# Kernel tuning notes

Hardware: AMD Instinct MI355X
Metric: run time of the kernel (lower is better)

Reference implementation:

```python
import jax, jax.numpy as jnp
import numpy as np

TOP_K = 2


def setup_inputs() -> dict:
    key = jax.random.key(0)
    k0, k1, k2, k3, k4 = jax.random.split(key, 5)
    B, S, D, E, F = 4, 2048, 1024, 8, 512
    return {
        "hidden_states": jax.random.normal(k0, (B, S, D), dtype=jnp.float32),
        "router_weight": jax.random.normal(k1, (E, D), dtype=jnp.float32) * 0.02,
        "w_gate": jax.random.normal(k2, (E, D, F), dtype=jnp.float32) * 0.02,
        "w_up": jax.random.normal(k3, (E, D, F), dtype=jnp.float32) * 0.02,
        "w_down": jax.random.normal(k4, (E, F, D), dtype=jnp.float32) * 0.02,
    }


def reference(hidden_states, router_weight, w_gate, w_up, w_down):
    B, S, D = hidden_states.shape
    E = router_weight.shape[0]
    x = hidden_states.reshape(-1, D)          # [T, D] token-flattened
    T = x.shape[0]

    # --- TopKRouter: softmax over experts, top-k, renormalize selected probs ---
    logits = x @ router_weight.T              # [T, E]
    probs = jax.nn.softmax(logits, axis=-1)
    top_p, top_i = jax.lax.top_k(probs, TOP_K)            # [T, k]
    top_p = top_p / jnp.sum(top_p, axis=-1, keepdims=True)  # renormalize=True

    # combine weights: scatter selected probabilities into [T, E]
    combine = jnp.zeros((T, E), x.dtype).at[jnp.arange(T)[:, None], top_i].add(top_p)

    # --- Grouped SwiGLU experts (dropless: zero combine weight => zero contribution) ---
    g = jnp.einsum('td,edf->tef', x, w_gate)  # [T, E, F]
    u = jnp.einsum('td,edf->tef', x, w_up)    # [T, E, F]
    h = jax.nn.silu(g) * u                    # SwiGLU activation
    # down-proj + weighted combine fused
    out = jnp.einsum('tef,efd,te->td', h, w_down, combine)  # [T, D]
    return out.reshape(B, S, D)
```

## Files before the change

kernel.cpp:

```cpp
#include <hip/hip_runtime.h>
#include <hip/hip_bf16.h>


typedef __attribute__((ext_vector_type(4))) float  f32x4;
typedef __attribute__((ext_vector_type(8))) unsigned short us8;
typedef __attribute__((ext_vector_type(4))) unsigned short us4;
typedef __bf16 bf16_t;
typedef __attribute__((ext_vector_type(8))) bf16_t bf16x8;

#define TTOK 8192
#define DDIM 1024
#define EEXP 8
#define FDIM 512

__device__ __forceinline__ unsigned short f2bf(float f) {
  unsigned int u = __float_as_uint(f);
  u = (u + 0x7FFFu + ((u >> 16) & 1u)) >> 16;
  return (unsigned short)u;
}

__device__ __forceinline__ void gload16(const void* g, void* l) {
  __builtin_amdgcn_global_load_lds(
      (const __attribute__((address_space(1))) void*)g,
      (__attribute__((address_space(3))) void*)l, 16, 0, 0);
}

__global__ __launch_bounds__(256) void k_cvt_x(const float* __restrict__ x,
                                               unsigned short* __restrict__ xb) {
  int i = blockIdx.x * 256 + threadIdx.x;
  const f32x4* s = (const f32x4*)x + (size_t)i * 2;
  f32x4 a = s[0], b = s[1];
  us8 o;
  o[0]=f2bf(a[0]); o[1]=f2bf(a[1]); o[2]=f2bf(a[2]); o[3]=f2bf(a[3]);
  o[4]=f2bf(b[0]); o[5]=f2bf(b[1]); o[6]=f2bf(b[2]); o[7]=f2bf(b[3]);
  *((us8*)xb + i) = o;
}

__global__ __launch_bounds__(256) void k_tcvt(const float* __restrict__ src,
                                              unsigned short* __restrict__ dst,
                                              int M, int N) {
  __shared__ float tile[32][33];
  int e  = blockIdx.z;
  int m0 = blockIdx.y * 32, n0 = blockIdx.x * 32;
  const float* s = src + (size_t)e * M * N;
  unsigned short* d = dst + (size_t)e * M * N;
  int r  = threadIdx.x >> 3;
  int c4 = (threadIdx.x & 7) * 4;
  f32x4 v = *(const f32x4*)(s + (size_t)(m0 + r) * N + n0 + c4);
  tile[r][c4+0] = v[0]; tile[r][c4+1] = v[1];
  tile[r][c4+2] = v[2]; tile[r][c4+3] = v[3];
  __syncthreads();
  us4 o;
  o[0] = f2bf(tile[c4+0][r]); o[1] = f2bf(tile[c4+1][r]);
  o[2] = f2bf(tile[c4+2][r]); o[3] = f2bf(tile[c4+3][r]);
  *(us4*)(d + (size_t)(n0 + r) * M + m0 + c4) = o;
}

__global__ __launch_bounds__(256) void k_router(const float* __restrict__ x,
                                                const float* __restrict__ rw,
                                                int* __restrict__ topki,
                                                float* __restrict__ topkw) {
  __shared__ float wlds[8 * 1024];
  int tid = threadIdx.x;
  #pragma unroll
  for (int i = 0; i < 8; ++i)
    ((f32x4*)wlds)[tid + i * 256] = ((const f32x4*)rw)[tid + i * 256];
  __syncthreads();

  int wv = tid >> 6, lane = tid & 63;
  int t = blockIdx.x * 4 + wv;
  const f32x4* xr = (const f32x4*)(x + (size_t)t * DDIM);
  f32x4 xv[4];
  #pragma unroll
  for (int j = 0; j < 4; ++j) xv[j] = xr[j * 64 + lane];
  double xd[16];
  #pragma unroll
  for (int j = 0; j < 4; ++j) {
    xd[j*4+0] = xv[j][0]; xd[j*4+1] = xv[j][1];
    xd[j*4+2] = xv[j][2]; xd[j*4+3] = xv[j][3];
  }
  float pf[8];
  #pragma unroll
  for (int e = 0; e < 8; ++e) {
    double acc = 0.0;
    #pragma unroll
    for (int j = 0; j < 4; ++j) {
      f32x4 wv4 = ((const f32x4*)(wlds + e * 1024))[j * 64 + lane];
      acc = fma((double)wv4[0], xd[j*4+0], acc);
      acc = fma((double)wv4[1], xd[j*4+1], acc);
      acc = fma((double)wv4[2], xd[j*4+2], acc);
      acc = fma((double)wv4[3], xd[j*4+3], acc);
    }
    pf[e] = (float)acc;
  }
  #pragma unroll
  for (int e = 0; e < 8; ++e) {
    #pragma unroll
    for (int off = 32; off >= 1; off >>= 1)
      pf[e] += __shfl_xor(pf[e], off, 64);
  }
  if (lane == 0) {
    int i1 = 0;
    #pragma unroll
    for (int e2 = 1; e2 < 8; ++e2) if (pf[e2] > pf[i1]) i1 = e2;
    int i2 = (i1 == 0) ? 1 : 0;
    #pragma unroll
    for (int e2 = 0; e2 < 8; ++e2) if (e2 != i1 && pf[e2] > pf[i2]) i2 = e2;
    float d21 = pf[i2] - pf[i1];
    float e1  = __expf(d21);
    float s   = 1.f + e1;
    topki[2*t]   = i1;       topki[2*t+1] = i2;
    topkw[2*t]   = 1.f / s;  topkw[2*t+1] = e1 / s;
  }
}

__global__ __launch_bounds__(256) void k_count(const int* __restrict__ topki,
                                               int* __restrict__ ctrs) {
  __shared__ int h[8];
  if (threadIdx.x < 8) h[threadIdx.x] = 0;
  __syncthreads();
  int i = blockIdx.x * 256 + threadIdx.x;
  atomicAdd(&h[topki[i]], 1);
  __syncthreads();
  if (threadIdx.x < 8) atomicAdd(&ctrs[threadIdx.x], h[threadIdx.x]);
}

__global__ void k_scan(int* __restrict__ ctrs) {
  if (threadIdx.x == 0 && blockIdx.x == 0) {
    ctrs[8] = 0;
    #pragma unroll
    for (int e = 0; e < 8; ++e) ctrs[9 + e] = ctrs[8 + e] + ctrs[e];
    #pragma unroll
    for (int e = 0; e < 8; ++e) ctrs[17 + e] = 0;
  }
}

__global__ __launch_bounds__(256) void k_scatter(const int* __restrict__ topki,
                                                 const float* __restrict__ topkw,
                                                 int* __restrict__ ctrs,
                                                 int* __restrict__ at,
                                                 float* __restrict__ aw) {
  __shared__ int lc[8], base[8];
  int tid = threadIdx.x;
  if (tid < 8) lc[tid] = 0;
  __syncthreads();
  int t = blockIdx.x * 256 + tid;
  int e0 = topki[2*t], e1 = topki[2*t+1];
  int r0 = atomicAdd(&lc[e0], 1);
  int r1 = atomicAdd(&lc[e1], 1);
  __syncthreads();
  if (tid < 8) base[tid] = atomicAdd(&ctrs[17 + tid], lc[tid]);
  __syncthreads();
  int a0 = ctrs[8 + e0] + base[e0] + r0;
  int a1 = ctrs[8 + e1] + base[e1] + r1;
  at[a0] = t; aw[a0] = topkw[2*t];
  at[a1] = t; aw[a1] = topkw[2*t+1];
}

__global__ __launch_bounds__(256) void k_gateup(
    const unsigned short* __restrict__ xb,
    const unsigned short* __restrict__ wgt,
    const unsigned short* __restrict__ wut,
    const int* __restrict__ at,
    const int* __restrict__ ctrs,
    unsigned short* __restrict__ h) {
  int e    = blockIdx.z;
  int seg0 = ctrs[8 + e];
  int cnt  = ctrs[9 + e] - seg0;
  int row0 = blockIdx.y * 128;
  if (row0 >= cnt) return;
  int f0 = blockIdx.x * 128;

  __shared__ unsigned short lA [128 * 64];
  __shared__ unsigned short lBg[128 * 64];
  __shared__ unsigned short lBu[128 * 64];
  __shared__ int s_tok[128];

  int tid = threadIdx.x;
  if (tid < 128) {
    int rg = row0 + tid;
    s_tok[tid] = at[seg0 + ((rg < cnt) ? rg : 0)];
  }
  __syncthreads();

  int a_row[4], a_su[4];
  const unsigned short* aSrc[4];
  size_t bOff[4];
  #pragma unroll
  for (int i = 0; i < 4; ++i) {
    a_row[i] = i * 32 + (tid >> 3);
    a_su[i]  = (tid & 7) ^ (a_row[i] & 7);
    aSrc[i]  = xb + (size_t)s_tok[a_row[i]] * DDIM + a_su[i] * 8;
    bOff[i]  = (size_t)a_row[i] * DDIM + a_su[i] * 8;
  }
  const unsigned short* bgBase = wgt + ((size_t)e * FDIM + f0) * DDIM;
  const unsigned short* buBase = wut + ((size_t)e * FDIM + f0) * DDIM;

  int w = tid >> 6, lane = tid & 63;
  int wr = (w >> 1) * 64, wc = (w & 1) * 64;

  f32x4 zero = {0.f, 0.f, 0.f, 0.f};
  f32x4 accg[4][4], accu[4][4];
  #pragma unroll
  for (int mt = 0; mt < 4; ++mt)
    #pragma unroll
    for (int nt = 0; nt < 4; ++nt) { accg[mt][nt] = zero; accu[mt][nt] = zero; }

  for (int ks = 0; ks < DDIM / 64; ++ks) {
    int k0 = ks * 64;
    #pragma unroll
    for (int i = 0; i < 4; ++i) {
      int dst = (i * 256 + tid) * 8;
      gload16(aSrc[i] + k0,          &lA [dst]);
      gload16(bgBase + bOff[i] + k0, &lBg[dst]);
      gload16(buBase + bOff[i] + k0, &lBu[dst]);
    }
    __syncthreads();
    #pragma unroll
    for (int kk = 0; kk < 2; ++kk) {
      bf16x8 af[4];
      #pragma unroll
      for (int mt = 0; mt < 4; ++mt) {
        int ar = wr + mt * 16 + (lane & 15);
        int au = (kk * 4 + (lane >> 4)) ^ (ar & 7);
        af[mt] = *(const bf16x8*)&lA[(ar * 8 + au) * 8];
      }
      #pragma unroll
      for (int nt = 0; nt < 4; ++nt) {
        int br = wc + nt * 16 + (lane & 15);
        int bu = (kk * 4 + (lane >> 4)) ^ (br & 7);
        bf16x8 bg = *(const bf16x8*)&lBg[(br * 8 + bu) * 8];
        bf16x8 bv = *(const bf16x8*)&lBu[(br * 8 + bu) * 8];
        #pragma unroll
        for (int mt = 0; mt < 4; ++mt) {
          accg[mt][nt] = __builtin_amdgcn_mfma_f32_16x16x32_bf16(af[mt], bg, accg[mt][nt], 0, 0, 0);
          accu[mt][nt] = __builtin_amdgcn_mfma_f32_16x16x32_bf16(af[mt], bv, accu[mt][nt], 0, 0, 0);
        }
      }
    }
    __syncthreads();
  }
  #pragma unroll
  for (int mt = 0; mt < 4; ++mt) {
    #pragma unroll
    for (int nt = 0; nt < 4; ++nt) {
      #pragma unroll
      for (int j = 0; j < 4; ++j) {
        int rl = wr + mt * 16 + (lane >> 4) * 4 + j;
        if (row0 + rl < cnt) {
          float g = accg[mt][nt][j], u = accu[mt][nt][j];
          float hv = g * (1.f / (1.f + __expf(-g))) * u;
          h[(size_t)(seg0 + row0 + rl) * FDIM + f0 + wc + nt * 16 + (lane & 15)] = f2bf(hv);
        }
      }
    }
  }
}

__global__ __launch_bounds__(256) void k_down(
    const unsigned short* __restrict__ h,
    const unsigned short* __restrict__ wdt,
    const int* __restrict__ at,
    const float* __restrict__ aw,
    const int* __restrict__ ctrs,
    float* __restrict__ out) {
  int e    = blockIdx.z;
  int seg0 = ctrs[8 + e];
  int cnt  = ctrs[9 + e] - seg0;
  int row0 = blockIdx.y * 128;
  if (row0 >= cnt) return;
  int d0 = blockIdx.x * 128;

  __shared__ unsigned short lA[128 * 64];
  __shared__ unsigned short lB[128 * 64];
  __shared__ int   s_tok[128];
  __shared__ float s_w[128];

  int tid = threadIdx.x;
  if (tid < 128) {
    int rg = row0 + tid;
    int a  = seg0 + ((rg < cnt) ? rg : 0);
    s_tok[tid] = at[a];
    s_w[tid]   = aw[a];
  }

  int a_row[4], a_su[4];
  const unsigned short* aSrc[4];
  size_t bOff[4];
  #pragma unroll
  for (int i = 0; i < 4; ++i) {
    a_row[i] = i * 32 + (tid >> 3);
    a_su[i]  = (tid & 7) ^ (a_row[i] & 7);
    int rr   = (row0 + a_row[i] < cnt) ? row0 + a_row[i] : 0;
    aSrc[i]  = h + (size_t)(seg0 + rr) * FDIM + a_su[i] * 8;
    bOff[i]  = (size_t)a_row[i] * FDIM + a_su[i] * 8;
  }
  const unsigned short* bBase = wdt + ((size_t)e * DDIM + d0) * FDIM;

  int w = tid >> 6, lane = tid & 63;
  int wr = (w >> 1) * 64, wc = (w & 1) * 64;

  f32x4 zero = {0.f, 0.f, 0.f, 0.f};
  f32x4 acc[4][4];
  #pragma unroll
  for (int mt = 0; mt < 4; ++mt)
    #pragma unroll
    for (int nt = 0; nt < 4; ++nt) acc[mt][nt] = zero;

  for (int ks = 0; ks < FDIM / 64; ++ks) {
    int k0 = ks * 64;
    #pragma unroll
    for (int i = 0; i < 4; ++i) {
      int dst = (i * 256 + tid) * 8;
      gload16(aSrc[i] + k0,         &lA[dst]);
      gload16(bBase + bOff[i] + k0, &lB[dst]);
    }
    __syncthreads();
    #pragma unroll
    for (int kk = 0; kk < 2; ++kk) {
      bf16x8 af[4];
      #pragma unroll
      for (int mt = 0; mt < 4; ++mt) {
        int ar = wr + mt * 16 + (lane & 15);
        int au = (kk * 4 + (lane >> 4)) ^ (ar & 7);
        af[mt] = *(const bf16x8*)&lA[(ar * 8 + au) * 8];
      }
      #pragma unroll
      for (int nt = 0; nt < 4; ++nt) {
        int br = wc + nt * 16 + (lane & 15);
        int bu = (kk * 4 + (lane >> 4)) ^ (br & 7);
        bf16x8 bf = *(const bf16x8*)&lB[(br * 8 + bu) * 8];
        #pragma unroll
        for (int mt = 0; mt < 4; ++mt)
          acc[mt][nt] = __builtin_amdgcn_mfma_f32_16x16x32_bf16(af[mt], bf, acc[mt][nt], 0, 0, 0);
      }
    }
    __syncthreads();
  }
  #pragma unroll
  for (int mt = 0; mt < 4; ++mt) {
    #pragma unroll
    for (int nt = 0; nt < 4; ++nt) {
      #pragma unroll
      for (int j = 0; j < 4; ++j) {
        int rl = wr + mt * 16 + (lane >> 4) * 4 + j;
        if (row0 + rl < cnt) {
          float v = acc[mt][nt][j] * s_w[rl];
          atomicAdd(out + (size_t)s_tok[rl] * DDIM + d0 + wc + nt * 16 + (lane & 15), v);
        }
      }
    }
  }
}

extern "C" void kernel_launch(void* const* d_in, const int* in_sizes, int n_in,
                              void* d_out, int out_size, void* d_ws, size_t ws_size,
                              hipStream_t stream) {
  (void)in_sizes; (void)n_in; (void)ws_size;
  const float* x  = (const float*)d_in[0];
  const float* rw = (const float*)d_in[1];
  const float* wg = (const float*)d_in[2];
  const float* wu = (const float*)d_in[3];
  const float* wd = (const float*)d_in[4];
  float* out = (float*)d_out;

  char* ws = (char*)d_ws;
  unsigned short* xb  = (unsigned short*)(ws + 0);
  unsigned short* wgt = (unsigned short*)(ws + 16777216);
  unsigned short* wut = (unsigned short*)(ws + 25165824);
  unsigned short* wdt = (unsigned short*)(ws + 33554432);
  unsigned short* hbuf= (unsigned short*)(ws + 41943040);
  float* topkw = (float*)(ws + 58720256);
  int*   topki = (int*)  (ws + 58785792);
  int*   at    = (int*)  (ws + 58851328);
  float* aw    = (float*)(ws + 58916864);
  int*   ctrs  = (int*)  (ws + 58982400);

  hipMemsetAsync(ctrs, 0, 256, stream);
  hipMemsetAsync(out, 0, (size_t)out_size * sizeof(float), stream);

  k_cvt_x<<<4096, 256, 0, stream>>>(x, xb);
  k_tcvt <<<dim3(16, 32, 8), 256, 0, stream>>>(wg, wgt, 1024, 512);
  k_tcvt <<<dim3(16, 32, 8), 256, 0, stream>>>(wu, wut, 1024, 512);
  k_tcvt <<<dim3(32, 16, 8), 256, 0, stream>>>(wd, wdt, 512, 1024);
  k_router<<<2048, 256, 0, stream>>>(x, rw, topki, topkw);
  k_count <<<64, 256, 0, stream>>>(topki, ctrs);
  k_scan  <<<1, 64, 0, stream>>>(ctrs);
  k_scatter<<<32, 256, 0, stream>>>(topki, topkw, ctrs, at, aw);
  k_gateup<<<dim3(4, 128, 8), 256, 0, stream>>>(xb, wgt, wut, at, ctrs, hbuf);
  k_down  <<<dim3(8, 128, 8), 256, 0, stream>>>(hbuf, wdt, at, aw, ctrs, out);
}
```

Baseline: 323.7 us.

## Double-buffer LDS and enlarge tiles in grouped MoE GEMM kernels

Both expert GEMM kernels now use 512-thread blocks with 256-row tiles (and 256-column tiles in the down projection), plus double-buffered LDS. The next K-slice is prefetched while the current one is computed, which removes one barrier per iteration and hides global-load latency. The larger tiles improve weight reuse across tokens. The cost is much higher LDS use (about 128KB per block in k_down), more accumulator registers per thread, lower occupancy and more wasted work on partially filled expert tiles.

After: 306.2 us. 5.4% less time.

```diff
diff --git a/kernel.cpp b/kernel.cpp
--- a/kernel.cpp
+++ b/kernel.cpp
@@ -157,7 +157,7 @@
   at[a1] = t; aw[a1] = topkw[2*t+1];
 }
 
-__global__ __launch_bounds__(256) void k_gateup(
+__global__ __launch_bounds__(512, 2) void k_gateup(
     const unsigned short* __restrict__ xb,
     const unsigned short* __restrict__ wgt,
     const unsigned short* __restrict__ wut,
@@ -167,31 +167,35 @@
   int e    = blockIdx.z;
   int seg0 = ctrs[8 + e];
   int cnt  = ctrs[9 + e] - seg0;
-  int row0 = blockIdx.y * 128;
+  int row0 = blockIdx.y * 256;
   if (row0 >= cnt) return;
   int f0 = blockIdx.x * 128;
 
-  __shared__ unsigned short lA [128 * 64];
-  __shared__ unsigned short lBg[128 * 64];
-  __shared__ unsigned short lBu[128 * 64];
-  __shared__ int s_tok[128];
+  __shared__ unsigned short lA [2][256 * 64];
+  __shared__ unsigned short lBg[2][128 * 64];
+  __shared__ unsigned short lBu[2][128 * 64];
+  __shared__ int s_tok[256];
 
   int tid = threadIdx.x;
-  if (tid < 128) {
+  if (tid < 256) {
     int rg = row0 + tid;
     s_tok[tid] = at[seg0 + ((rg < cnt) ? rg : 0)];
   }
   __syncthreads();
 
-  int a_row[4], a_su[4];
   const unsigned short* aSrc[4];
-  size_t bOff[4];
+  size_t bOff[2];
   #pragma unroll
   for (int i = 0; i < 4; ++i) {
-    a_row[i] = i * 32 + (tid >> 3);
-    a_su[i]  = (tid & 7) ^ (a_row[i] & 7);
-    aSrc[i]  = xb + (size_t)s_tok[a_row[i]] * DDIM + a_su[i] * 8;
-    bOff[i]  = (size_t)a_row[i] * DDIM + a_su[i] * 8;
+    int row = i * 64 + (tid >> 3);
+    int su  = (tid & 7) ^ (row & 7);
+    aSrc[i] = xb + (size_t)s_tok[row] * DDIM + su * 8;
+  }
+  #pragma unroll
+  for (int j = 0; j < 2; ++j) {
+    int row = j * 64 + (tid >> 3);
+    int su  = (tid & 7) ^ (row & 7);
+    bOff[j] = (size_t)row * DDIM + su * 8;
   }
   const unsigned short* bgBase = wgt + ((size_t)e * FDIM + f0) * DDIM;
   const unsigned short* buBase = wut + ((size_t)e * FDIM + f0) * DDIM;
@@ -206,16 +210,28 @@
     #pragma unroll
     for (int nt = 0; nt < 4; ++nt) { accg[mt][nt] = zero; accu[mt][nt] = zero; }
 
+  #pragma unroll
+  for (int i = 0; i < 4; ++i) gload16(aSrc[i], &lA[0][(i * 512 + tid) * 8]);
+  #pragma unroll
+  for (int j = 0; j < 2; ++j) {
+    gload16(bgBase + bOff[j], &lBg[0][(j * 512 + tid) * 8]);
+    gload16(buBase + bOff[j], &lBu[0][(j * 512 + tid) * 8]);
+  }
+  __syncthreads();
+
+  int cur = 0;
   for (int ks = 0; ks < DDIM / 64; ++ks) {
-    int k0 = ks * 64;
-    #pragma unroll
-    for (int i = 0; i < 4; ++i) {
-      int dst = (i * 256 + tid) * 8;
-      gload16(aSrc[i] + k0,          &lA [dst]);
-      gload16(bgBase + bOff[i] + k0, &lBg[dst]);
-      gload16(buBase + bOff[i] + k0, &lBu[dst]);
-    }
-    __syncthreads();
+    if (ks + 1 < DDIM / 64) {
+      int k1 = (ks + 1) * 64;
+      int nx = cur ^ 1;
+      #pragma unroll
+      for (int i = 0; i < 4; ++i) gload16(aSrc[i] + k1, &lA[nx][(i * 512 + tid) * 8]);
+      #pragma unroll
+      for (int j = 0; j < 2; ++j) {
+        gload16(bgBase + bOff[j] + k1, &lBg[nx][(j * 512 + tid) * 8]);
+        gload16(buBase + bOff[j] + k1, &lBu[nx][(j * 512 + tid) * 8]);
+      }
+    }
     #pragma unroll
     for (int kk = 0; kk < 2; ++kk) {
       bf16x8 af[4];
@@ -223,14 +239,14 @@
       for (int mt = 0; mt < 4; ++mt) {
         int ar = wr + mt * 16 + (lane & 15);
         int au = (kk * 4 + (lane >> 4)) ^ (ar & 7);
-        af[mt] = *(const bf16x8*)&lA[(ar * 8 + au) * 8];
+        af[mt] = *(const bf16x8*)&lA[cur][(ar * 8 + au) * 8];
       }
       #pragma unroll
       for (int nt = 0; nt < 4; ++nt) {
         int br = wc + nt * 16 + (lane & 15);
         int bu = (kk * 4 + (lane >> 4)) ^ (br & 7);
-        bf16x8 bg = *(const bf16x8*)&lBg[(br * 8 + bu) * 8];
-        bf16x8 bv = *(const bf16x8*)&lBu[(br * 8 + bu) * 8];
+        bf16x8 bg = *(const bf16x8*)&lBg[cur][(br * 8 + bu) * 8];
+        bf16x8 bv = *(const bf16x8*)&lBu[cur][(br * 8 + bu) * 8];
         #pragma unroll
         for (int mt = 0; mt < 4; ++mt) {
           accg[mt][nt] = __builtin_amdgcn_mfma_f32_16x16x32_bf16(af[mt], bg, accg[mt][nt], 0, 0, 0);
@@ -239,6 +255,7 @@
       }
     }
     __syncthreads();
+    cur ^= 1;
   }
   #pragma unroll
   for (int mt = 0; mt < 4; ++mt) {
@@ -257,7 +274,7 @@
   }
 }
 
-__global__ __launch_bounds__(256) void k_down(
+__global__ __launch_bounds__(512, 2) void k_down(
     const unsigned short* __restrict__ h,
     const unsigned short* __restrict__ wdt,
     const int* __restrict__ at,
@@ -267,55 +284,64 @@
   int e    = blockIdx.z;
   int seg0 = ctrs[8 + e];
   int cnt  = ctrs[9 + e] - seg0;
-  int row0 = blockIdx.y * 128;
+  int row0 = blockIdx.y * 256;
   if (row0 >= cnt) return;
-  int d0 = blockIdx.x * 128;
-
-  __shared__ unsigned short lA[128 * 64];
-  __shared__ unsigned short lB[128 * 64];
-  __shared__ int   s_tok[128];
-  __shared__ float s_w[128];
+  int d0 = blockIdx.x * 256;
+
+  __shared__ unsigned short lA[2][256 * 64];
+  __shared__ unsigned short lB[2][256 * 64];
+  __shared__ int   s_tok[256];
+  __shared__ float s_w[256];
 
   int tid = threadIdx.x;
-  if (tid < 128) {
+  if (tid < 256) {
     int rg = row0 + tid;
     int a  = seg0 + ((rg < cnt) ? rg : 0);
     s_tok[tid] = at[a];
     s_w[tid]   = aw[a];
   }
-
-  int a_row[4], a_su[4];
+  __syncthreads();
+
   const unsigned short* aSrc[4];
   size_t bOff[4];
   #pragma unroll
   for (int i = 0; i < 4; ++i) {
-    a_row[i] = i * 32 + (tid >> 3);
-    a_su[i]  = (tid & 7) ^ (a_row[i] & 7);
-    int rr   = (row0 + a_row[i] < cnt) ? row0 + a_row[i] : 0;
-    aSrc[i]  = h + (size_t)(seg0 + rr) * FDIM + a_su[i] * 8;
-    bOff[i]  = (size_t)a_row[i] * FDIM + a_su[i] * 8;
+    int row = i * 64 + (tid >> 3);
+    int su  = (tid & 7) ^ (row & 7);
+    int rr  = (row0 + row < cnt) ? row0 + row : 0;
+    aSrc[i] = h + (size_t)(seg0 + rr) * FDIM + su * 8;
+    bOff[i] = (size_t)row * FDIM + su * 8;
   }
   const unsigned short* bBase = wdt + ((size_t)e * DDIM + d0) * FDIM;
 
   int w = tid >> 6, lane = tid & 63;
-  int wr = (w >> 1) * 64, wc = (w & 1) * 64;
+  int wr = (w >> 1) * 64, wc = (w & 1) * 128;
 
   f32x4 zero = {0.f, 0.f, 0.f, 0.f};
-  f32x4 acc[4][4];
+  f32x4 acc[4][8];
   #pragma unroll
   for (int mt = 0; mt < 4; ++mt)
     #pragma unroll
-    for (int nt = 0; nt < 4; ++nt) acc[mt][nt] = zero;
-
+    for (int nt = 0; nt < 8; ++nt) acc[mt][nt] = zero;
+
+  #pragma unroll
+  for (int i = 0; i < 4; ++i) {
+    gload16(aSrc[i],         &lA[0][(i * 512 + tid) * 8]);
+    gload16(bBase + bOff[i], &lB[0][(i * 512 + tid) * 8]);
+  }
+  __syncthreads();
+
+  int cur = 0;
   for (int ks = 0; ks < FDIM / 64; ++ks) {
-    int k0 = ks * 64;
-    #pragma unroll
-    for (int i = 0; i < 4; ++i) {
-      int dst = (i * 256 + tid) * 8;
-      gload16(aSrc[i] + k0,         &lA[dst]);
-      gload16(bBase + bOff[i] + k0, &lB[dst]);
-    }
-    __syncthreads();
+    if (ks + 1 < FDIM / 64) {
+      int k1 = (ks + 1) * 64;
+      int nx = cur ^ 1;
+      #pragma unroll
+      for (int i = 0; i < 4; ++i) {
+        gload16(aSrc[i] + k1,         &lA[nx][(i * 512 + tid) * 8]);
+        gload16(bBase + bOff[i] + k1, &lB[nx][(i * 512 + tid) * 8]);
+      }
+    }
     #pragma unroll
     for (int kk = 0; kk < 2; ++kk) {
       bf16x8 af[4];
@@ -323,24 +349,25 @@
       for (int mt = 0; mt < 4; ++mt) {
         int ar = wr + mt * 16 + (lane & 15);
         int au = (kk * 4 + (lane >> 4)) ^ (ar & 7);
-        af[mt] = *(const bf16x8*)&lA[(ar * 8 + au) * 8];
-      }
-      #pragma unroll
-      for (int nt = 0; nt < 4; ++nt) {
+        af[mt] = *(const bf16x8*)&lA[cur][(ar * 8 + au) * 8];
+      }
+      #pragma unroll
+      for (int nt = 0; nt < 8; ++nt) {
         int br = wc + nt * 16 + (lane & 15);
         int bu = (kk * 4 + (lane >> 4)) ^ (br & 7);
-        bf16x8 bf = *(const bf16x8*)&lB[(br * 8 + bu) * 8];
+        bf16x8 bf = *(const bf16x8*)&lB[cur][(br * 8 + bu) * 8];
         #pragma unroll
         for (int mt = 0; mt < 4; ++mt)
           acc[mt][nt] = __builtin_amdgcn_mfma_f32_16x16x32_bf16(af[mt], bf, acc[mt][nt], 0, 0, 0);
       }
     }
     __syncthreads();
+    cur ^= 1;
   }
   #pragma unroll
   for (int mt = 0; mt < 4; ++mt) {
     #pragma unroll
-    for (int nt = 0; nt < 4; ++nt) {
+    for (int nt = 0; nt < 8; ++nt) {
       #pragma unroll
       for (int j = 0; j < 4; ++j) {
         int rl = wr + mt * 16 + (lane >> 4) * 4 + j;
@@ -387,6 +414,6 @@
   k_count <<<64, 256, 0, stream>>>(topki, ctrs);
   k_scan  <<<1, 64, 0, stream>>>(ctrs);
   k_scatter<<<32, 256, 0, stream>>>(topki, topkw, ctrs, at, aw);
-  k_gateup<<<dim3(4, 128, 8), 256, 0, stream>>>(xb, wgt, wut, at, ctrs, hbuf);
-  k_down  <<<dim3(8, 128, 8), 256, 0, stream>>>(hbuf, wdt, at, aw, ctrs, out);
-}
+  k_gateup<<<dim3(4, 64, 8), 512, 0, stream>>>(xb, wgt, wut, at, ctrs, hbuf);
+  k_down  <<<dim3(4, 64, 8), 512, 0, stream>>>(hbuf, wdt, at, aw, ctrs, out);
+}
```
